# Kernel optimization log

Hardware: AMD Instinct MI355X
Metric: run time of the kernel (lower is better)

## Reference

```python
import jax, jax.numpy as jnp
import numpy as np

N_QUBITS = 9
N_LAYERS = 5
NUM_CLASSES = 10
BATCH = 4096
TWO_PI = 6.283185307179586


def _rx(theta):
    # RX(theta) = [[cos(t/2), -i sin(t/2)], [-i sin(t/2), cos(t/2)]]; theta scalar -> [2,2], [B] -> [B,2,2]
    c = jnp.cos(theta / 2).astype(jnp.complex64)
    s = ((-1j) * jnp.sin(theta / 2)).astype(jnp.complex64)
    return jnp.stack([jnp.stack([c, s], -1), jnp.stack([s, c], -1)], -2)


def _rot(phi, theta, omega):
    # PennyLane Rot = RZ(omega) @ RY(theta) @ RZ(phi)
    ct = jnp.cos(theta / 2)
    st = jnp.sin(theta / 2)
    a = jnp.exp(-0.5j * (phi + omega)) * ct
    b = -jnp.exp(0.5j * (phi - omega)) * st
    c = jnp.exp(-0.5j * (phi - omega)) * st
    d = jnp.exp(0.5j * (phi + omega)) * ct
    return jnp.stack([jnp.stack([a, b]), jnp.stack([c, d])]).astype(jnp.complex64)


def _apply1(state, gate, w):
    # state: [B] + [2]*9 (wire w lives on axis 1+w, wire 0 most significant as in PennyLane)
    s = jnp.moveaxis(state, 1 + w, -1)
    if gate.ndim == 3:  # per-sample gate (AngleEmbedding)
        s = jnp.einsum('bij,b...j->b...i', gate, s)
    else:
        s = jnp.einsum('ij,...j->...i', gate, s)
    return jnp.moveaxis(s, -1, 1 + w)


def _apply_crx(state, theta, ctrl, tgt):
    g = _rx(theta)  # [2,2]
    s = jnp.moveaxis(state, (1 + ctrl, 1 + tgt), (-2, -1))
    s1 = jnp.einsum('ij,...j->...i', g, s[..., 1, :])  # RX applied only where control bit = 1
    s = jnp.concatenate([s[..., :1, :], s1[..., None, :]], axis=-2)
    return jnp.moveaxis(s, (-2, -1), (1 + ctrl, 1 + tgt))


def _circuit(x, rot_w, crx_w):
    B = x.shape[0]
    state = jnp.zeros((B,) + (2,) * N_QUBITS, jnp.complex64)
    state = state.at[(slice(None),) + (0,) * N_QUBITS].set(1.0)  # |0...0>
    for n in range(N_LAYERS):
        for w in range(N_QUBITS):  # AngleEmbedding (RX) with per-sample angles
            state = _apply1(state, _rx(x[:, w]), w)
        for w in range(N_QUBITS):  # Rot gates
            state = _apply1(state, _rot(rot_w[n, w, 0], rot_w[n, w, 1], rot_w[n, w, 2]), w)
        for w in range(N_QUBITS):  # CRX ring entanglers
            state = _apply_crx(state, crx_w[n, w, 0], w, (w + 1) % N_QUBITS)
    probs = state.real ** 2 + state.imag ** 2  # [B] + [2]*9
    evs = []
    for w in range(N_QUBITS):
        other = tuple(a for a in range(1, N_QUBITS + 1) if a != 1 + w)
        p = probs.sum(axis=other)  # [B, 2]
        evs.append(p[:, 0] - p[:, 1])  # <Z_w>
    return jnp.stack(evs, axis=-1)  # [B, 9]


def setup_inputs() -> dict:
    key = jax.random.key(0)
    k0, k1, k2, k3 = jax.random.split(key, 4)
    x = jax.random.normal(k0, (BATCH, N_QUBITS), dtype=jnp.float32)
    rot_w = jax.random.uniform(k1, (N_LAYERS, N_QUBITS, 3), dtype=jnp.float32, minval=0.0, maxval=TWO_PI)
    crx_w = jax.random.uniform(k2, (N_LAYERS, N_QUBITS, 1), dtype=jnp.float32, minval=0.0, maxval=TWO_PI)
    fc_w = jax.random.normal(k3, (NUM_CLASSES, N_QUBITS), dtype=jnp.float32) * (1.0 / 3.0)
    fc_b = jnp.zeros((NUM_CLASSES,), dtype=jnp.float32)
    return {"x": x, "rot_w": rot_w, "crx_w": crx_w, "fc_w": fc_w, "fc_b": fc_b}


def reference(x, rot_w, crx_w, fc_w, fc_b):
    evs = _circuit(x, rot_w, crx_w)            # [B, 9] PauliZ expectation values
    logits = evs @ fc_w.T + fc_b               # [B, num_classes]
    return jax.nn.log_softmax(logits, axis=1)
```

## Files before the change

### kernel.cpp

```cpp
#include <hip/hip_runtime.h>
#include <math.h>

#define NQ 9
#define NL 5
#define NC 10

typedef float v2f __attribute__((ext_vector_type(2)));
typedef float v4f __attribute__((ext_vector_type(4)));

__device__ __forceinline__ v2f sp(float x) { v2f r; r.x = x; r.y = x; return r; }

__device__ __forceinline__ void plswap(float& a, float& b, int mask) {
    if (mask == 32) {
        auto r = __builtin_amdgcn_permlane32_swap(__float_as_int(a), __float_as_int(b), false, false);
        a = __int_as_float(r[0]); b = __int_as_float(r[1]);
    } else {
        auto r = __builtin_amdgcn_permlane16_swap(__float_as_int(a), __float_as_int(b), false, false);
        a = __int_as_float(r[0]); b = __int_as_float(r[1]);
    }
}
__device__ __forceinline__ void plswap2(v2f& a, v2f& b, int mask) {
    float ax = a.x, bx = b.x, ay = a.y, by = b.y;
    plswap(ax, bx, mask); plswap(ay, by, mask);
    a.x = ax; a.y = ay; b.x = bx; b.y = by;
}
__device__ __forceinline__ void state_swap(v2f (&xr)[4], v2f (&xi)[4], int mask) {
    plswap2(xr[0], xr[1], mask); plswap2(xr[2], xr[3], mask);
    plswap2(xi[0], xi[1], mask); plswap2(xi[2], xi[3], mask);
}

__device__ __forceinline__ void swpm(float x, int mask, float& hi, float& lo) {
    if (mask == 32) {
        auto r = __builtin_amdgcn_permlane32_swap(__float_as_int(x), __float_as_int(x), false, false);
        lo = __int_as_float(r[0]); hi = __int_as_float(r[1]);
    } else {
        auto r = __builtin_amdgcn_permlane16_swap(__float_as_int(x), __float_as_int(x), false, false);
        lo = __int_as_float(r[0]); hi = __int_as_float(r[1]);
    }
}

__device__ __forceinline__ float xmove(float x, int mask) {
    if (mask == 1)
        return __int_as_float(__builtin_amdgcn_update_dpp(0, __float_as_int(x), 0xB1, 0xF, 0xF, true));
    if (mask == 2)
        return __int_as_float(__builtin_amdgcn_update_dpp(0, __float_as_int(x), 0x4E, 0xF, 0xF, true));
    if (mask == 4) {
        int t = __builtin_amdgcn_update_dpp(0, __float_as_int(x), 0x104, 0xF, 0x5, false);
        t = __builtin_amdgcn_update_dpp(t, __float_as_int(x), 0x114, 0xF, 0xA, false);
        return __int_as_float(t);
    }
    return __int_as_float(__builtin_amdgcn_update_dpp(0, __float_as_int(x), 0x128, 0xF, 0xF, true));
}
__device__ __forceinline__ v2f xmv2(v2f v, int mask) {
    v2f r; r.x = xmove(v.x, mask); r.y = xmove(v.y, mask); return r;
}


#define HALF_U(A, c, s)                                               \
    float u00r = A.x*c + s*A.w,  u00i = A.y*c - s*A.z;                \
    float u01r = A.z*c + s*A.y,  u01i = A.w*c - s*A.x;

__device__ __forceinline__ void rot_pair(v2f (&xr)[4], v2f (&xi)[4],
                                         const float* __restrict__ m, float c, float s) {
    const v4f A = *(const v4f*)m;
    HALF_U(A, c, s)
#pragma unroll
    for (int p = 0; p < 4; p += 2) {
        const int q = p + 1;
        v2f a0r = xr[p], a0i = xi[p], a1r = xr[q], a1i = xi[q];
        xr[p] = sp(u00r)*a0r - sp(u00i)*a0i + sp(u01r)*a1r - sp(u01i)*a1i;
        xi[p] = sp(u00r)*a0i + sp(u00i)*a0r + sp(u01r)*a1i + sp(u01i)*a1r;
        xr[q] = sp(-u01r)*a0r - sp(u01i)*a0i + sp(u00r)*a1r + sp(u00i)*a1i;
        xi[q] = sp(-u01r)*a0i + sp(u01i)*a0r + sp(u00r)*a1i - sp(u00i)*a1r;
    }
}

template<int CB, int LB>
__device__ __forceinline__ void fusedC_cross(v2f (&xr)[4], v2f (&xi)[4],
                                             const float* __restrict__ m,
                                             float c, float s, int lane) {
    const v4f A0 = *(const v4f*)m;
    const v4f A1 = *(const v4f*)(m + 4);
    const bool ctrl = (lane >> CB) & 1;
    v4f A;
    A.x = ctrl ? A1.x : A0.x;  A.y = ctrl ? A1.y : A0.y;
    A.z = ctrl ? A1.z : A0.z;  A.w = ctrl ? A1.w : A0.w;
    HALF_U(A, c, s)
    const int bit = (lane >> LB) & 1;
    const float Csr = u00r,  Cpi = u01i;
    const float Csi = bit ? -u00i : u00i;
    const float Cpr = bit ? -u01r : u01r;
#pragma unroll
    for (int j = 0; j < 4; ++j) {
        v2f pr = xmv2(xr[j], 1 << LB);
        v2f pi = xmv2(xi[j], 1 << LB);
        v2f ar = xr[j], ai = xi[j];
        xr[j] = sp(Csr)*ar - sp(Csi)*ai + sp(Cpr)*pr - sp(Cpi)*pi;
        xi[j] = sp(Csr)*ai + sp(Csi)*ar + sp(Cpr)*pi + sp(Cpi)*pr;
    }
}

__device__ __forceinline__ void fusedC_j1(v2f (&xr)[4], v2f (&xi)[4],
                                          const float* __restrict__ m,
                                          float c, float s, int lane) {
    const v4f A0 = *(const v4f*)m;
    const v4f A1 = *(const v4f*)(m + 4);
    const bool ctrl = lane & 1;
    v4f A;
    A.x = ctrl ? A1.x : A0.x;  A.y = ctrl ? A1.y : A0.y;
    A.z = ctrl ? A1.z : A0.z;  A.w = ctrl ? A1.w : A0.w;
    HALF_U(A, c, s)
#pragma unroll
    for (int j = 0; j < 2; ++j) {
        const int q = j | 2;
        v2f a0r = xr[j], a0i = xi[j], a1r = xr[q], a1i = xi[q];
        xr[j] = sp(u00r)*a0r - sp(u00i)*a0i + sp(u01r)*a1r - sp(u01i)*a1i;
        xi[j] = sp(u00r)*a0i + sp(u00i)*a0r + sp(u01r)*a1i + sp(u01i)*a1r;
        xr[q] = sp(-u01r)*a0r - sp(u01i)*a0i + sp(u00r)*a1r + sp(u00i)*a1i;
        xi[q] = sp(-u01r)*a0i + sp(u01i)*a0r + sp(u00r)*a1i - sp(u00i)*a1r;
    }
}

__device__ __forceinline__ void rot_comp(v2f (&xr)[4], v2f (&xi)[4],
                                         const float* __restrict__ m, float c, float s) {
    const v4f A = *(const v4f*)m;
    HALF_U(A, c, s)
    v2f U0r = { u00r, -u01r }, U0i = { u00i,  u01i };
    v2f U1r = { u01r,  u00r }, U1i = { u01i, -u00i };
#pragma unroll
    for (int j = 0; j < 4; ++j) {
        v2f A0r = xr[j].xx, A0i = xi[j].xx, A1r = xr[j].yy, A1i = xi[j].yy;
        xr[j] = U0r*A0r - U0i*A0i + U1r*A1r - U1i*A1i;
        xi[j] = U0r*A0i + U0i*A0r + U1r*A1i + U1i*A1r;
    }
}

template<int CB, int M>
__device__ __forceinline__ void crx_dpp(v2f (&xr)[4], v2f (&xi)[4], float c, float s, int lane) {
    const bool ctrl = (lane >> CB) & 1;
    const float ce = ctrl ? c : 1.f;
    const float se = ctrl ? s : 0.f;
#pragma unroll
    for (int j = 0; j < 4; ++j) {
        v2f pr = xmv2(xr[j], M);
        v2f pi = xmv2(xi[j], M);
        xr[j] = sp(ce)*xr[j] + sp(se)*pi;
        xi[j] = sp(ce)*xi[j] - sp(se)*pr;
    }
}
__device__ __forceinline__ void crx_pair_s(v2f (&xr)[4], v2f (&xi)[4], float ce, float se) {
#pragma unroll
    for (int p = 0; p < 4; p += 2) {
        const int q = p + 1;
        v2f a0r = xr[p], a0i = xi[p], a1r = xr[q], a1i = xi[q];
        xr[p] = sp(ce)*a0r + sp(se)*a1i;
        xi[p] = sp(ce)*a0i - sp(se)*a1r;
        xr[q] = sp(ce)*a1r + sp(se)*a0i;
        xi[q] = sp(ce)*a1i - sp(se)*a0r;
    }
}
__device__ __forceinline__ void crx_pair_c(v2f (&xr)[4], v2f (&xi)[4], float c, float s) {
    const v2f cev = {1.f, c};
    const v2f sev = {0.f, s};
#pragma unroll
    for (int p = 0; p < 4; p += 2) {
        const int q = p + 1;
        v2f a0r = xr[p], a0i = xi[p], a1r = xr[q], a1i = xi[q];
        xr[p] = cev*a0r + sev*a1i;
        xi[p] = cev*a0i - sev*a1r;
        xr[q] = cev*a1r + sev*a0i;
        xi[q] = cev*a1i - sev*a0r;
    }
}
__device__ __forceinline__ void crx_l_j1(v2f (&xr)[4], v2f (&xi)[4], float c, float s, int lane) {
    const bool ctrl = lane & 1;
    const float ce = ctrl ? c : 1.f;
    const float se = ctrl ? s : 0.f;
#pragma unroll
    for (int j = 0; j < 2; ++j) {
        const int q = j | 2;
        v2f a0r = xr[j], a0i = xi[j], a1r = xr[q], a1i = xi[q];
        xr[j] = sp(ce)*a0r + sp(se)*a1i;
        xi[j] = sp(ce)*a0i - sp(se)*a1r;
        xr[q] = sp(ce)*a1r + sp(se)*a0i;
        xi[q] = sp(ce)*a1i - sp(se)*a0r;
    }
}
__device__ __forceinline__ void crx_j1_j0(v2f (&xr)[4], v2f (&xi)[4], float c, float s) {
    v2f a0r = xr[2], a0i = xi[2], a1r = xr[3], a1i = xi[3];
    xr[2] = sp(c)*a0r + sp(s)*a1i;
    xi[2] = sp(c)*a0i - sp(s)*a1r;
    xr[3] = sp(c)*a1r + sp(s)*a0i;
    xi[3] = sp(c)*a1i - sp(s)*a0r;
}
__device__ __forceinline__ void crx_j0_c(v2f (&xr)[4], v2f (&xi)[4], float c, float s) {
#pragma unroll
    for (int j = 1; j < 4; j += 2) {
        v2f vr = xr[j], vi = xi[j];
        xr[j] = sp(c)*vr + sp(s)*vi.yx;
        xi[j] = sp(c)*vi - sp(s)*vr.yx;
    }
}

__global__ __launch_bounds__(256) void qmlp_kernel(
    const float* __restrict__ x, const float* __restrict__ rot_w,
    const float* __restrict__ crx_w, const float* __restrict__ fc_w,
    const float* __restrict__ fc_b, float* __restrict__ out, int B)
{
    __shared__ __align__(16) float rotm[NL * NQ * 8];
    __shared__ __align__(16) float crxm[NL * NQ * 2];
    __shared__ float fcw[NC * NQ];
    __shared__ float fcbs[NC];

    const int tid = threadIdx.x;
    if (tid < NL * NQ) {
        const int n = tid / NQ, w = tid % NQ;
        const float phi = rot_w[tid * 3 + 0];
        const float th  = rot_w[tid * 3 + 1];
        const float om  = rot_w[tid * 3 + 2];
        float st, ct; sincosf(0.5f * th, &st, &ct);
        float spo, cpo; sincosf(0.5f * (phi + om), &spo, &cpo);
        float smo, cmo; sincosf(0.5f * (phi - om), &smo, &cmo);
        const float m00r =  ct * cpo, m00i = -ct * spo;
        const float m01r = -st * cmo, m01i = -st * smo;
        float* m = rotm + tid * 8;
        m[0] = m00r; m[1] = m00i; m[2] = m01r; m[3] = m01i;
        const int nb = n * NQ + (w + NQ - 1) % NQ;
        float sq, cq; sincosf(0.5f * crx_w[nb], &sq, &cq);
        m[4] = cq*m00r + sq*m01i;
        m[5] = cq*m00i + sq*m01r;
        m[6] = cq*m01r - sq*m00i;
        m[7] = cq*m01i - sq*m00r;
        float sc, cc; sincosf(0.5f * crx_w[tid], &sc, &cc);
        crxm[tid * 2 + 0] = cc; crxm[tid * 2 + 1] = sc;
    }
    if (tid < NC * NQ) fcw[tid] = fc_w[tid];
    if (tid < NC) fcbs[tid] = fc_b[tid];
    __syncthreads();

    const int lane = tid & 63;
    const int b = blockIdx.x * 4 + (tid >> 6);
    if (b >= B) return;

    float cx[NQ], sx[NQ];
#pragma unroll
    for (int w = 0; w < NQ; ++w) __sincosf(0.5f * x[b * NQ + w], &sx[w], &cx[w]);

    v2f xr[4], xi[4];

    {
        const float* M = rotm;
        float ar = 1.f, ai = 0.f;
#pragma unroll
        for (int w = 0; w < 6; ++w) {
            const v4f A = *(const v4f*)(M + w * 8);
            float c = cx[w], s = sx[w];
            HALF_U(A, c, s)
            int bit = (lane >> (5 - w)) & 1;
            float vr = bit ? -u01r : u00r;
            float vi = bit ?  u01i : u00i;
            float nr = ar * vr - ai * vi;
            float ni = ar * vi + ai * vr;
            ar = nr; ai = ni;
        }
        float vr67[2][2], vi67[2][2];
#pragma unroll
        for (int q = 0; q < 2; ++q) {
            const v4f A = *(const v4f*)(M + (6 + q) * 8);
            float c = cx[6 + q], s = sx[6 + q];
            HALF_U(A, c, s)
            vr67[q][0] = u00r;  vi67[q][0] = u00i;
            vr67[q][1] = -u01r; vi67[q][1] = u01i;
        }
        float t6r[2], t6i[2];
#pragma unroll
        for (int bb = 0; bb < 2; ++bb) {
            t6r[bb] = ar * vr67[0][bb] - ai * vi67[0][bb];
            t6i[bb] = ar * vi67[0][bb] + ai * vr67[0][bb];
        }
        float t67r[4], t67i[4];
#pragma unroll
        for (int j = 0; j < 4; ++j) {
            int b6 = j >> 1, b7 = j & 1;
            t67r[j] = t6r[b6] * vr67[1][b7] - t6i[b6] * vi67[1][b7];
            t67i[j] = t6r[b6] * vi67[1][b7] + t6i[b6] * vr67[1][b7];
        }
        {
            const v4f A = *(const v4f*)(M + 8 * 8);
            float c = cx[8], s = sx[8];
            HALF_U(A, c, s)
            v2f V8r = { u00r, -u01r };
            v2f V8i = { u00i,  u01i };
#pragma unroll
            for (int j = 0; j < 4; ++j) {
                xr[j] = sp(t67r[j])*V8r - sp(t67i[j])*V8i;
                xi[j] = sp(t67r[j])*V8i + sp(t67i[j])*V8r;
            }
        }
    }

    {
        const float* C = crxm;
        state_swap(xr, xi, 16);
        {
            const bool ctrl = (lane >> 5) & 1;
            crx_pair_s(xr, xi, ctrl ? C[0] : 1.f, ctrl ? C[1] : 0.f);
        }
        state_swap(xr, xi, 16);
        crx_dpp<4, 8>(xr, xi, C[2],  C[3],  lane);
        crx_dpp<3, 4>(xr, xi, C[4],  C[5],  lane);
        crx_dpp<2, 2>(xr, xi, C[6],  C[7],  lane);
        crx_dpp<1, 1>(xr, xi, C[8],  C[9],  lane);
        crx_l_j1     (xr, xi, C[10], C[11], lane);
        crx_j1_j0    (xr, xi, C[12], C[13]);
        crx_j0_c     (xr, xi, C[14], C[15]);
        state_swap(xr, xi, 32);
        crx_pair_c(xr, xi, C[16], C[17]);
    }

    for (int n = 1; n < NL; ++n) {
        const float* M = rotm + n * NQ * 8;
        const float* C = crxm + n * NQ * 2;
        rot_pair(xr, xi, M + 0 * 8, cx[0], sx[0]);
        state_swap(xr, xi, 32);
        state_swap(xr, xi, 16);
        rot_pair(xr, xi, M + 1 * 8, cx[1], sx[1]);
        {
            const bool ctrl = (lane >> 5) & 1;
            crx_pair_s(xr, xi, ctrl ? C[0] : 1.f, ctrl ? C[1] : 0.f);
        }
        state_swap(xr, xi, 16);
        fusedC_cross<4, 3>(xr, xi, M + 2 * 8, cx[2], sx[2], lane);
        fusedC_cross<3, 2>(xr, xi, M + 3 * 8, cx[3], sx[3], lane);
        fusedC_cross<2, 1>(xr, xi, M + 4 * 8, cx[4], sx[4], lane);
        fusedC_cross<1, 0>(xr, xi, M + 5 * 8, cx[5], sx[5], lane);
        fusedC_j1(xr, xi, M + 6 * 8, cx[6], sx[6], lane);
        rot_pair(xr, xi, M + 7 * 8, cx[7], sx[7]);
        crx_j1_j0(xr, xi, C[12], C[13]);
        rot_comp(xr, xi, M + 8 * 8, cx[8], sx[8]);
        crx_j0_c(xr, xi, C[14], C[15]);
        state_swap(xr, xi, 32);
        crx_pair_c(xr, xi, C[16], C[17]);
    }
    state_swap(xr, xi, 32);

    v2f P[4];
#pragma unroll
    for (int j = 0; j < 4; ++j) P[j] = xr[j]*xr[j] + xi[j]*xi[j];
    float ps[4];
#pragma unroll
    for (int j = 0; j < 4; ++j) ps[j] = P[j].x + P[j].y;
    float psum = ps[0] + ps[1] + ps[2] + ps[3];

    float t = psum;
    float d[6];
#pragma unroll
    for (int bb = 0; bb < 6; ++bb) {
        if (bb < 4) {
#pragma unroll
            for (int jj = 0; jj < 6; ++jj)
                if (jj < bb) d[jj] += xmove(d[jj], 1 << bb);
            float o = xmove(t, 1 << bb);
            d[bb] = ((lane >> bb) & 1) ? (o - t) : (t - o);
            t += o;
        } else {
#pragma unroll
            for (int jj = 0; jj < 6; ++jj)
                if (jj < bb) { float h, l; swpm(d[jj], 1 << bb, h, l); d[jj] = h + l; }
            float h, l; swpm(t, 1 << bb, h, l);
            d[bb] = l - h;
            t = h + l;
        }
    }
    float e6 = (ps[0] + ps[1]) - (ps[2] + ps[3]);
    float e7 = (ps[0] + ps[2]) - (ps[1] + ps[3]);
    float e8 = (P[0].x - P[0].y) + (P[1].x - P[1].y)
             + (P[2].x - P[2].y) + (P[3].x - P[3].y);
#pragma unroll
    for (int m = 1; m < 16; m <<= 1) {
        e6 += xmove(e6, m); e7 += xmove(e7, m); e8 += xmove(e8, m);
    }
    {
        float h, l;
        swpm(e6, 16, h, l); e6 = h + l;  swpm(e6, 32, h, l); e6 = h + l;
        swpm(e7, 16, h, l); e7 = h + l;  swpm(e7, 32, h, l); e7 = h + l;
        swpm(e8, 16, h, l); e8 = h + l;  swpm(e8, 32, h, l); e8 = h + l;
    }

    float ev[NQ];
#pragma unroll
    for (int w = 0; w < 6; ++w) ev[w] = d[5 - w];
    ev[6] = e6; ev[7] = e7; ev[8] = e8;

    float lval = -INFINITY;
    if (lane < NC) {
        float dd = fcbs[lane];
        const float* fw = fcw + lane * NQ;
#pragma unroll
        for (int w = 0; w < NQ; ++w) dd += ev[w] * fw[w];
        lval = dd;
    }
    float mx = lval;
    mx = fmaxf(mx, xmove(mx, 1));
    mx = fmaxf(mx, xmove(mx, 2));
    mx = fmaxf(mx, xmove(mx, 4));
    mx = fmaxf(mx, xmove(mx, 8));
    float e = (lane < NC) ? expf(lval - mx) : 0.f;
    float se = e;
    se += xmove(se, 1); se += xmove(se, 2); se += xmove(se, 4); se += xmove(se, 8);
    if (lane < NC) out[b * NC + lane] = lval - mx - logf(se);
}

extern "C" void kernel_launch(void* const* d_in, const int* in_sizes, int n_in,
                              void* d_out, int out_size, void* d_ws, size_t ws_size,
                              hipStream_t stream) {
    const float* x     = (const float*)d_in[0];
    const float* rot_w = (const float*)d_in[1];
    const float* crx_w = (const float*)d_in[2];
    const float* fc_w  = (const float*)d_in[3];
    const float* fc_b  = (const float*)d_in[4];
    float* out = (float*)d_out;
    const int B = in_sizes[0] / NQ;
    const int blocks = (B + 3) / 4;
    qmlp_kernel<<<blocks, 256, 0, stream>>>(x, rot_w, crx_w, fc_w, fc_b, out, B);
}
```

Before: 31.06 us.

## Process two batch samples per wavefront with interleaved state updates

Each wavefront now simulates two independent samples, keeping two register-resident state vectors and interleaving their gate, swap and reduction steps. The grid is halved to match. The aim is more instruction-level parallelism to hide DPP/permlane and ALU latency, and to amortise the per-block shared-memory setup over more samples. In exchange it doubles register pressure, which may lower occupancy, and leaves half as many wavefronts on the GPU. When B is odd, x is read out of bounds for the second sample (b1) even though its output write is guarded.

Result: no change. 30.88 us (-0.6%).

```diff
diff --git a/kernel.cpp b/kernel.cpp
--- a/kernel.cpp
+++ b/kernel.cpp
@@ -54,7 +54,6 @@
 __device__ __forceinline__ v2f xmv2(v2f v, int mask) {
     v2f r; r.x = xmove(v.x, mask); r.y = xmove(v.y, mask); return r;
 }
-
 
 #define HALF_U(A, c, s)                                               \
     float u00r = A.x*c + s*A.w,  u00i = A.y*c - s*A.z;                \
@@ -199,6 +198,57 @@
         v2f vr = xr[j], vi = xi[j];
         xr[j] = sp(c)*vr + sp(s)*vi.yx;
         xi[j] = sp(c)*vi - sp(s)*vr.yx;
+    }
+}
+
+__device__ __forceinline__ void init_state(v2f (&xr)[4], v2f (&xi)[4],
+                                           const float* __restrict__ M,
+                                           const float (&cx)[NQ], const float (&sx)[NQ],
+                                           int lane) {
+    float ar = 1.f, ai = 0.f;
+#pragma unroll
+    for (int w = 0; w < 6; ++w) {
+        const v4f A = *(const v4f*)(M + w * 8);
+        float c = cx[w], s = sx[w];
+        HALF_U(A, c, s)
+        int bit = (lane >> (5 - w)) & 1;
+        float vr = bit ? -u01r : u00r;
+        float vi = bit ?  u01i : u00i;
+        float nr = ar * vr - ai * vi;
+        float ni = ar * vi + ai * vr;
+        ar = nr; ai = ni;
+    }
+    float vr67[2][2], vi67[2][2];
+#pragma unroll
+    for (int q = 0; q < 2; ++q) {
+        const v4f A = *(const v4f*)(M + (6 + q) * 8);
+        float c = cx[6 + q], s = sx[6 + q];
+        HALF_U(A, c, s)
+        vr67[q][0] = u00r;  vi67[q][0] = u00i;
+        vr67[q][1] = -u01r; vi67[q][1] = u01i;
+    }
+    float t6r[2], t6i[2];
+#pragma unroll
+    for (int bb = 0; bb < 2; ++bb) {
+        t6r[bb] = ar * vr67[0][bb] - ai * vi67[0][bb];
+        t6i[bb] = ar * vi67[0][bb] + ai * vr67[0][bb];
+    }
+    float t67r[4], t67i[4];
+#pragma unroll
+    for (int j = 0; j < 4; ++j) {
+        int b6 = j >> 1, b7 = j & 1;
+        t67r[j] = t6r[b6] * vr67[1][b7] - t6i[b6] * vi67[1][b7];
+        t67i[j] = t6r[b6] * vi67[1][b7] + t6i[b6] * vr67[1][b7];
+    }
+    const v4f A = *(const v4f*)(M + 8 * 8);
+    float c = cx[8], s = sx[8];
+    HALF_U(A, c, s)
+    v2f V8r = { u00r, -u01r };
+    v2f V8i = { u00i,  u01i };
+#pragma unroll
+    for (int j = 0; j < 4; ++j) {
+        xr[j] = sp(t67r[j])*V8r - sp(t67i[j])*V8i;
+        xi[j] = sp(t67r[j])*V8i + sp(t67i[j])*V8r;
     }
 }
 
@@ -239,176 +289,179 @@
     __syncthreads();
 
     const int lane = tid & 63;
-    const int b = blockIdx.x * 4 + (tid >> 6);
-    if (b >= B) return;
-
-    float cx[NQ], sx[NQ];
-#pragma unroll
-    for (int w = 0; w < NQ; ++w) __sincosf(0.5f * x[b * NQ + w], &sx[w], &cx[w]);
-
-    v2f xr[4], xi[4];
-
-    {
-        const float* M = rotm;
-        float ar = 1.f, ai = 0.f;
-#pragma unroll
-        for (int w = 0; w < 6; ++w) {
-            const v4f A = *(const v4f*)(M + w * 8);
-            float c = cx[w], s = sx[w];
-            HALF_U(A, c, s)
-            int bit = (lane >> (5 - w)) & 1;
-            float vr = bit ? -u01r : u00r;
-            float vi = bit ?  u01i : u00i;
-            float nr = ar * vr - ai * vi;
-            float ni = ar * vi + ai * vr;
-            ar = nr; ai = ni;
-        }
-        float vr67[2][2], vi67[2][2];
-#pragma unroll
-        for (int q = 0; q < 2; ++q) {
-            const v4f A = *(const v4f*)(M + (6 + q) * 8);
-            float c = cx[6 + q], s = sx[6 + q];
-            HALF_U(A, c, s)
-            vr67[q][0] = u00r;  vi67[q][0] = u00i;
-            vr67[q][1] = -u01r; vi67[q][1] = u01i;
-        }
-        float t6r[2], t6i[2];
-#pragma unroll
-        for (int bb = 0; bb < 2; ++bb) {
-            t6r[bb] = ar * vr67[0][bb] - ai * vi67[0][bb];
-            t6i[bb] = ar * vi67[0][bb] + ai * vr67[0][bb];
-        }
-        float t67r[4], t67i[4];
-#pragma unroll
-        for (int j = 0; j < 4; ++j) {
-            int b6 = j >> 1, b7 = j & 1;
-            t67r[j] = t6r[b6] * vr67[1][b7] - t6i[b6] * vi67[1][b7];
-            t67i[j] = t6r[b6] * vi67[1][b7] + t6i[b6] * vr67[1][b7];
-        }
-        {
-            const v4f A = *(const v4f*)(M + 8 * 8);
-            float c = cx[8], s = sx[8];
-            HALF_U(A, c, s)
-            v2f V8r = { u00r, -u01r };
-            v2f V8i = { u00i,  u01i };
-#pragma unroll
-            for (int j = 0; j < 4; ++j) {
-                xr[j] = sp(t67r[j])*V8r - sp(t67i[j])*V8i;
-                xi[j] = sp(t67r[j])*V8i + sp(t67i[j])*V8r;
-            }
-        }
-    }
+    const int b0 = (blockIdx.x * 4 + (tid >> 6)) * 2;
+    const int b1 = b0 + 1;
+    if (b0 >= B) return;
+
+    float cxA[NQ], sxA[NQ], cxB[NQ], sxB[NQ];
+#pragma unroll
+    for (int w = 0; w < NQ; ++w) __sincosf(0.5f * x[b0 * NQ + w], &sxA[w], &cxA[w]);
+#pragma unroll
+    for (int w = 0; w < NQ; ++w) __sincosf(0.5f * x[b1 * NQ + w], &sxB[w], &cxB[w]);
+
+    v2f xrA[4], xiA[4], xrB[4], xiB[4];
+    init_state(xrA, xiA, rotm, cxA, sxA, lane);
+    init_state(xrB, xiB, rotm, cxB, sxB, lane);
 
     {
         const float* C = crxm;
-        state_swap(xr, xi, 16);
+        state_swap(xrA, xiA, 16);
+        state_swap(xrB, xiB, 16);
         {
             const bool ctrl = (lane >> 5) & 1;
-            crx_pair_s(xr, xi, ctrl ? C[0] : 1.f, ctrl ? C[1] : 0.f);
+            const float ce = ctrl ? C[0] : 1.f, se = ctrl ? C[1] : 0.f;
+            crx_pair_s(xrA, xiA, ce, se);
+            crx_pair_s(xrB, xiB, ce, se);
         }
-        state_swap(xr, xi, 16);
-        crx_dpp<4, 8>(xr, xi, C[2],  C[3],  lane);
-        crx_dpp<3, 4>(xr, xi, C[4],  C[5],  lane);
-        crx_dpp<2, 2>(xr, xi, C[6],  C[7],  lane);
-        crx_dpp<1, 1>(xr, xi, C[8],  C[9],  lane);
-        crx_l_j1     (xr, xi, C[10], C[11], lane);
-        crx_j1_j0    (xr, xi, C[12], C[13]);
-        crx_j0_c     (xr, xi, C[14], C[15]);
-        state_swap(xr, xi, 32);
-        crx_pair_c(xr, xi, C[16], C[17]);
+        state_swap(xrA, xiA, 16);
+        state_swap(xrB, xiB, 16);
+        crx_dpp<4, 8>(xrA, xiA, C[2],  C[3],  lane);  crx_dpp<4, 8>(xrB, xiB, C[2],  C[3],  lane);
+        crx_dpp<3, 4>(xrA, xiA, C[4],  C[5],  lane);  crx_dpp<3, 4>(xrB, xiB, C[4],  C[5],  lane);
+        crx_dpp<2, 2>(xrA, xiA, C[6],  C[7],  lane);  crx_dpp<2, 2>(xrB, xiB, C[6],  C[7],  lane);
+        crx_dpp<1, 1>(xrA, xiA, C[8],  C[9],  lane);  crx_dpp<1, 1>(xrB, xiB, C[8],  C[9],  lane);
+        crx_l_j1     (xrA, xiA, C[10], C[11], lane);  crx_l_j1     (xrB, xiB, C[10], C[11], lane);
+        crx_j1_j0    (xrA, xiA, C[12], C[13]);        crx_j1_j0    (xrB, xiB, C[12], C[13]);
+        crx_j0_c     (xrA, xiA, C[14], C[15]);        crx_j0_c     (xrB, xiB, C[14], C[15]);
+        state_swap(xrA, xiA, 32);
+        state_swap(xrB, xiB, 32);
+        crx_pair_c(xrA, xiA, C[16], C[17]);
+        crx_pair_c(xrB, xiB, C[16], C[17]);
     }
 
     for (int n = 1; n < NL; ++n) {
         const float* M = rotm + n * NQ * 8;
         const float* C = crxm + n * NQ * 2;
-        rot_pair(xr, xi, M + 0 * 8, cx[0], sx[0]);
-        state_swap(xr, xi, 32);
-        state_swap(xr, xi, 16);
-        rot_pair(xr, xi, M + 1 * 8, cx[1], sx[1]);
+        rot_pair(xrA, xiA, M + 0 * 8, cxA[0], sxA[0]);
+        rot_pair(xrB, xiB, M + 0 * 8, cxB[0], sxB[0]);
+        state_swap(xrA, xiA, 32);
+        state_swap(xrB, xiB, 32);
+        state_swap(xrA, xiA, 16);
+        state_swap(xrB, xiB, 16);
+        rot_pair(xrA, xiA, M + 1 * 8, cxA[1], sxA[1]);
+        rot_pair(xrB, xiB, M + 1 * 8, cxB[1], sxB[1]);
         {
             const bool ctrl = (lane >> 5) & 1;
-            crx_pair_s(xr, xi, ctrl ? C[0] : 1.f, ctrl ? C[1] : 0.f);
+            const float ce = ctrl ? C[0] : 1.f, se = ctrl ? C[1] : 0.f;
+            crx_pair_s(xrA, xiA, ce, se);
+            crx_pair_s(xrB, xiB, ce, se);
         }
-        state_swap(xr, xi, 16);
-        fusedC_cross<4, 3>(xr, xi, M + 2 * 8, cx[2], sx[2], lane);
-        fusedC_cross<3, 2>(xr, xi, M + 3 * 8, cx[3], sx[3], lane);
-        fusedC_cross<2, 1>(xr, xi, M + 4 * 8, cx[4], sx[4], lane);
-        fusedC_cross<1, 0>(xr, xi, M + 5 * 8, cx[5], sx[5], lane);
-        fusedC_j1(xr, xi, M + 6 * 8, cx[6], sx[6], lane);
-        rot_pair(xr, xi, M + 7 * 8, cx[7], sx[7]);
-        crx_j1_j0(xr, xi, C[12], C[13]);
-        rot_comp(xr, xi, M + 8 * 8, cx[8], sx[8]);
-        crx_j0_c(xr, xi, C[14], C[15]);
-        state_swap(xr, xi, 32);
-        crx_pair_c(xr, xi, C[16], C[17]);
-    }
-    state_swap(xr, xi, 32);
-
-    v2f P[4];
-#pragma unroll
-    for (int j = 0; j < 4; ++j) P[j] = xr[j]*xr[j] + xi[j]*xi[j];
-    float ps[4];
-#pragma unroll
-    for (int j = 0; j < 4; ++j) ps[j] = P[j].x + P[j].y;
-    float psum = ps[0] + ps[1] + ps[2] + ps[3];
-
-    float t = psum;
-    float d[6];
+        state_swap(xrA, xiA, 16);
+        state_swap(xrB, xiB, 16);
+        fusedC_cross<4, 3>(xrA, xiA, M + 2 * 8, cxA[2], sxA[2], lane);
+        fusedC_cross<4, 3>(xrB, xiB, M + 2 * 8, cxB[2], sxB[2], lane);
+        fusedC_cross<3, 2>(xrA, xiA, M + 3 * 8, cxA[3], sxA[3], lane);
+        fusedC_cross<3, 2>(xrB, xiB, M + 3 * 8, cxB[3], sxB[3], lane);
+        fusedC_cross<2, 1>(xrA, xiA, M + 4 * 8, cxA[4], sxA[4], lane);
+        fusedC_cross<2, 1>(xrB, xiB, M + 4 * 8, cxB[4], sxB[4], lane);
+        fusedC_cross<1, 0>(xrA, xiA, M + 5 * 8, cxA[5], sxA[5], lane);
+        fusedC_cross<1, 0>(xrB, xiB, M + 5 * 8, cxB[5], sxB[5], lane);
+        fusedC_j1(xrA, xiA, M + 6 * 8, cxA[6], sxA[6], lane);
+        fusedC_j1(xrB, xiB, M + 6 * 8, cxB[6], sxB[6], lane);
+        rot_pair(xrA, xiA, M + 7 * 8, cxA[7], sxA[7]);
+        rot_pair(xrB, xiB, M + 7 * 8, cxB[7], sxB[7]);
+        crx_j1_j0(xrA, xiA, C[12], C[13]);
+        crx_j1_j0(xrB, xiB, C[12], C[13]);
+        rot_comp(xrA, xiA, M + 8 * 8, cxA[8], sxA[8]);
+        rot_comp(xrB, xiB, M + 8 * 8, cxB[8], sxB[8]);
+        crx_j0_c(xrA, xiA, C[14], C[15]);
+        crx_j0_c(xrB, xiB, C[14], C[15]);
+        state_swap(xrA, xiA, 32);
+        state_swap(xrB, xiB, 32);
+        crx_pair_c(xrA, xiA, C[16], C[17]);
+        crx_pair_c(xrB, xiB, C[16], C[17]);
+    }
+    state_swap(xrA, xiA, 32);
+    state_swap(xrB, xiB, 32);
+
+    v2f PA[4], PB[4];
+#pragma unroll
+    for (int j = 0; j < 4; ++j) { PA[j] = xrA[j]*xrA[j] + xiA[j]*xiA[j];
+                                  PB[j] = xrB[j]*xrB[j] + xiB[j]*xiB[j]; }
+    float psA[4], psB[4];
+#pragma unroll
+    for (int j = 0; j < 4; ++j) { psA[j] = PA[j].x + PA[j].y; psB[j] = PB[j].x + PB[j].y; }
+    float tA = psA[0] + psA[1] + psA[2] + psA[3];
+    float tB = psB[0] + psB[1] + psB[2] + psB[3];
+
+    float dA[6], dB[6];
 #pragma unroll
     for (int bb = 0; bb < 6; ++bb) {
         if (bb < 4) {
 #pragma unroll
             for (int jj = 0; jj < 6; ++jj)
-                if (jj < bb) d[jj] += xmove(d[jj], 1 << bb);
-            float o = xmove(t, 1 << bb);
-            d[bb] = ((lane >> bb) & 1) ? (o - t) : (t - o);
-            t += o;
+                if (jj < bb) { dA[jj] += xmove(dA[jj], 1 << bb); dB[jj] += xmove(dB[jj], 1 << bb); }
+            float oA = xmove(tA, 1 << bb);
+            float oB = xmove(tB, 1 << bb);
+            bool hibit = (lane >> bb) & 1;
+            dA[bb] = hibit ? (oA - tA) : (tA - oA);
+            dB[bb] = hibit ? (oB - tB) : (tB - oB);
+            tA += oA; tB += oB;
         } else {
 #pragma unroll
             for (int jj = 0; jj < 6; ++jj)
-                if (jj < bb) { float h, l; swpm(d[jj], 1 << bb, h, l); d[jj] = h + l; }
-            float h, l; swpm(t, 1 << bb, h, l);
-            d[bb] = l - h;
-            t = h + l;
+                if (jj < bb) {
+                    float h, l;
+                    swpm(dA[jj], 1 << bb, h, l); dA[jj] = h + l;
+                    swpm(dB[jj], 1 << bb, h, l); dB[jj] = h + l;
+                }
+            float hA, lA, hB, lB;
+            swpm(tA, 1 << bb, hA, lA);
+            swpm(tB, 1 << bb, hB, lB);
+            dA[bb] = lA - hA; tA = hA + lA;
+            dB[bb] = lB - hB; tB = hB + lB;
         }
     }
-    float e6 = (ps[0] + ps[1]) - (ps[2] + ps[3]);
-    float e7 = (ps[0] + ps[2]) - (ps[1] + ps[3]);
-    float e8 = (P[0].x - P[0].y) + (P[1].x - P[1].y)
-             + (P[2].x - P[2].y) + (P[3].x - P[3].y);
+    float e6A = (psA[0] + psA[1]) - (psA[2] + psA[3]);
+    float e7A = (psA[0] + psA[2]) - (psA[1] + psA[3]);
+    float e8A = (PA[0].x - PA[0].y) + (PA[1].x - PA[1].y) + (PA[2].x - PA[2].y) + (PA[3].x - PA[3].y);
+    float e6B = (psB[0] + psB[1]) - (psB[2] + psB[3]);
+    float e7B = (psB[0] + psB[2]) - (psB[1] + psB[3]);
+    float e8B = (PB[0].x - PB[0].y) + (PB[1].x - PB[1].y) + (PB[2].x - PB[2].y) + (PB[3].x - PB[3].y);
 #pragma unroll
     for (int m = 1; m < 16; m <<= 1) {
-        e6 += xmove(e6, m); e7 += xmove(e7, m); e8 += xmove(e8, m);
+        e6A += xmove(e6A, m); e7A += xmove(e7A, m); e8A += xmove(e8A, m);
+        e6B += xmove(e6B, m); e7B += xmove(e7B, m); e8B += xmove(e8B, m);
     }
     {
         float h, l;
-        swpm(e6, 16, h, l); e6 = h + l;  swpm(e6, 32, h, l); e6 = h + l;
-        swpm(e7, 16, h, l); e7 = h + l;  swpm(e7, 32, h, l); e7 = h + l;
-        swpm(e8, 16, h, l); e8 = h + l;  swpm(e8, 32, h, l); e8 = h + l;
-    }
-
-    float ev[NQ];
-#pragma unroll
-    for (int w = 0; w < 6; ++w) ev[w] = d[5 - w];
-    ev[6] = e6; ev[7] = e7; ev[8] = e8;
-
-    float lval = -INFINITY;
+        swpm(e6A, 16, h, l); e6A = h + l;  swpm(e6A, 32, h, l); e6A = h + l;
+        swpm(e7A, 16, h, l); e7A = h + l;  swpm(e7A, 32, h, l); e7A = h + l;
+        swpm(e8A, 16, h, l); e8A = h + l;  swpm(e8A, 32, h, l); e8A = h + l;
+        swpm(e6B, 16, h, l); e6B = h + l;  swpm(e6B, 32, h, l); e6B = h + l;
+        swpm(e7B, 16, h, l); e7B = h + l;  swpm(e7B, 32, h, l); e7B = h + l;
+        swpm(e8B, 16, h, l); e8B = h + l;  swpm(e8B, 32, h, l); e8B = h + l;
+    }
+
+    float evA[NQ], evB[NQ];
+#pragma unroll
+    for (int w = 0; w < 6; ++w) { evA[w] = dA[5 - w]; evB[w] = dB[5 - w]; }
+    evA[6] = e6A; evA[7] = e7A; evA[8] = e8A;
+    evB[6] = e6B; evB[7] = e7B; evB[8] = e8B;
+
+    float lvA = -INFINITY, lvB = -INFINITY;
     if (lane < NC) {
-        float dd = fcbs[lane];
+        float a = fcbs[lane], c2 = a;
         const float* fw = fcw + lane * NQ;
 #pragma unroll
-        for (int w = 0; w < NQ; ++w) dd += ev[w] * fw[w];
-        lval = dd;
-    }
-    float mx = lval;
-    mx = fmaxf(mx, xmove(mx, 1));
-    mx = fmaxf(mx, xmove(mx, 2));
-    mx = fmaxf(mx, xmove(mx, 4));
-    mx = fmaxf(mx, xmove(mx, 8));
-    float e = (lane < NC) ? expf(lval - mx) : 0.f;
-    float se = e;
-    se += xmove(se, 1); se += xmove(se, 2); se += xmove(se, 4); se += xmove(se, 8);
-    if (lane < NC) out[b * NC + lane] = lval - mx - logf(se);
+        for (int w = 0; w < NQ; ++w) { a += evA[w] * fw[w]; c2 += evB[w] * fw[w]; }
+        lvA = a; lvB = c2;
+    }
+    float mxA = lvA, mxB = lvB;
+    mxA = fmaxf(mxA, xmove(mxA, 1)); mxB = fmaxf(mxB, xmove(mxB, 1));
+    mxA = fmaxf(mxA, xmove(mxA, 2)); mxB = fmaxf(mxB, xmove(mxB, 2));
+    mxA = fmaxf(mxA, xmove(mxA, 4)); mxB = fmaxf(mxB, xmove(mxB, 4));
+    mxA = fmaxf(mxA, xmove(mxA, 8)); mxB = fmaxf(mxB, xmove(mxB, 8));
+    float eA = (lane < NC) ? expf(lvA - mxA) : 0.f;
+    float eB = (lane < NC) ? expf(lvB - mxB) : 0.f;
+    float seA = eA, seB = eB;
+    seA += xmove(seA, 1); seB += xmove(seB, 1);
+    seA += xmove(seA, 2); seB += xmove(seB, 2);
+    seA += xmove(seA, 4); seB += xmove(seB, 4);
+    seA += xmove(seA, 8); seB += xmove(seB, 8);
+    if (lane < NC) {
+        out[b0 * NC + lane] = lvA - mxA - logf(seA);
+        if (b1 < B) out[b1 * NC + lane] = lvB - mxB - logf(seB);
+    }
 }
 
 extern "C" void kernel_launch(void* const* d_in, const int* in_sizes, int n_in,
@@ -421,6 +474,7 @@
     const float* fc_b  = (const float*)d_in[4];
     float* out = (float*)d_out;
     const int B = in_sizes[0] / NQ;
-    const int blocks = (B + 3) / 4;
+    const int nw = (B + 1) / 2;
+    const int blocks = (nw + 3) / 4;
     qmlp_kernel<<<blocks, 256, 0, stream>>>(x, rot_w, crx_w, fc_w, fc_b, out, B);
 }
```

## Fold CRX gates into adjacent rotation matrices via precomputed dual matrices

Applied to the files above, without the earlier changes.

Removes separate CRX passes inside the layer loop by folding them into neighbouring rotation gates. It uses dual (control-selected) precomputed matrices for wires 1, 7 and 8, and merges the last CRX of the previous layer into the next layer's first RX angle. This cuts the per-layer VALU work and register shuffles for the state. The change relies on a host- or setup-side precompute of the doubled rotation matrices (m+4 slots) for those wires, and on RX angle composition holding per control half. If that precompute does not exist, the results will be wrong.

New measurement: 30.17 us. 2.9% less time.

```diff
diff --git a/kernel.cpp b/kernel.cpp
--- a/kernel.cpp
+++ b/kernel.cpp
@@ -55,23 +55,78 @@
     v2f r; r.x = xmove(v.x, mask); r.y = xmove(v.y, mask); return r;
 }
 
-
 #define HALF_U(A, c, s)                                               \
     float u00r = A.x*c + s*A.w,  u00i = A.y*c - s*A.z;                \
     float u01r = A.z*c + s*A.y,  u01i = A.w*c - s*A.x;
 
-__device__ __forceinline__ void rot_pair(v2f (&xr)[4], v2f (&xi)[4],
-                                         const float* __restrict__ m, float c, float s) {
+#define PAIR_BODY(p, q)                                                       \
+    {                                                                         \
+        v2f a0r = xr[p], a0i = xi[p], a1r = xr[q], a1i = xi[q];               \
+        xr[p] = sp(u00r)*a0r - sp(u00i)*a0i + sp(u01r)*a1r - sp(u01i)*a1i;    \
+        xi[p] = sp(u00r)*a0i + sp(u00i)*a0r + sp(u01r)*a1i + sp(u01i)*a1r;    \
+        xr[q] = sp(-u01r)*a0r - sp(u01i)*a0i + sp(u00r)*a1r + sp(u00i)*a1i;   \
+        xi[q] = sp(-u01r)*a0i + sp(u01i)*a0r + sp(u00r)*a1i - sp(u00i)*a1r;   \
+    }
+
+__device__ __forceinline__ void rot_pair_dual(v2f (&xr)[4], v2f (&xi)[4],
+                                              const float* __restrict__ m, float c, float s) {
+    const v4f A0 = *(const v4f*)m;
+    const v4f A1 = *(const v4f*)(m + 4);
+    { HALF_U(A0, c, s) PAIR_BODY(0, 1) }
+    { HALF_U(A1, c, s) PAIR_BODY(2, 3) }
+}
+
+__device__ __forceinline__ void rot_pair_sel(v2f (&xr)[4], v2f (&xi)[4],
+                                             const float* __restrict__ m, float c, float s,
+                                             bool ctrl) {
+    const v4f A0 = *(const v4f*)m;
+    const v4f A1 = *(const v4f*)(m + 4);
+    v4f A;
+    A.x = ctrl ? A1.x : A0.x;  A.y = ctrl ? A1.y : A0.y;
+    A.z = ctrl ? A1.z : A0.z;  A.w = ctrl ? A1.w : A0.w;
+    HALF_U(A, c, s)
+    PAIR_BODY(0, 1)
+    PAIR_BODY(2, 3)
+}
+
+__device__ __forceinline__ void rot_pair_v2(v2f (&xr)[4], v2f (&xi)[4],
+                                            const float* __restrict__ m, v2f c, v2f s) {
     const v4f A = *(const v4f*)m;
-    HALF_U(A, c, s)
+    v2f u00r = sp(A.x)*c + s*sp(A.w);
+    v2f u00i = sp(A.y)*c - s*sp(A.z);
+    v2f u01r = sp(A.z)*c + s*sp(A.y);
+    v2f u01i = sp(A.w)*c - s*sp(A.x);
 #pragma unroll
     for (int p = 0; p < 4; p += 2) {
         const int q = p + 1;
         v2f a0r = xr[p], a0i = xi[p], a1r = xr[q], a1i = xi[q];
-        xr[p] = sp(u00r)*a0r - sp(u00i)*a0i + sp(u01r)*a1r - sp(u01i)*a1i;
-        xi[p] = sp(u00r)*a0i + sp(u00i)*a0r + sp(u01r)*a1i + sp(u01i)*a1r;
-        xr[q] = sp(-u01r)*a0r - sp(u01i)*a0i + sp(u00r)*a1r + sp(u00i)*a1i;
-        xi[q] = sp(-u01r)*a0i + sp(u01i)*a0r + sp(u00r)*a1i - sp(u00i)*a1r;
+        xr[p] = u00r*a0r - u00i*a0i + u01r*a1r - u01i*a1i;
+        xi[p] = u00r*a0i + u00i*a0r + u01r*a1i + u01i*a1r;
+        xr[q] = -u01r*a0r - u01i*a0i + u00r*a1r + u00i*a1i;
+        xi[q] = -u01r*a0i + u01i*a0r + u00r*a1i - u00i*a1r;
+    }
+}
+
+__device__ __forceinline__ void rot_comp_dual(v2f (&xr)[4], v2f (&xi)[4],
+                                              const float* __restrict__ m, float c, float s) {
+    const v4f A0v = *(const v4f*)m;
+    const v4f A1v = *(const v4f*)(m + 4);
+    v2f U0r0, U0i0, U1r0, U1i0, U0r1, U0i1, U1r1, U1i1;
+    { HALF_U(A0v, c, s)
+      U0r0 = (v2f){ u00r, -u01r }; U0i0 = (v2f){ u00i,  u01i };
+      U1r0 = (v2f){ u01r,  u00r }; U1i0 = (v2f){ u01i, -u00i }; }
+    { HALF_U(A1v, c, s)
+      U0r1 = (v2f){ u00r, -u01r }; U0i1 = (v2f){ u00i,  u01i };
+      U1r1 = (v2f){ u01r,  u00r }; U1i1 = (v2f){ u01i, -u00i }; }
+#pragma unroll
+    for (int j = 0; j < 4; ++j) {
+        v2f U0r = (j & 1) ? U0r1 : U0r0;
+        v2f U0i = (j & 1) ? U0i1 : U0i0;
+        v2f U1r = (j & 1) ? U1r1 : U1r0;
+        v2f U1i = (j & 1) ? U1i1 : U1i0;
+        v2f A0r = xr[j].xx, A0i = xi[j].xx, A1r = xr[j].yy, A1i = xi[j].yy;
+        xr[j] = U0r*A0r - U0i*A0i + U1r*A1r - U1i*A1i;
+        xi[j] = U0r*A0i + U0i*A0r + U1r*A1i + U1i*A1r;
     }
 }
 
@@ -118,20 +173,6 @@
         xi[j] = sp(u00r)*a0i + sp(u00i)*a0r + sp(u01r)*a1i + sp(u01i)*a1r;
         xr[q] = sp(-u01r)*a0r - sp(u01i)*a0i + sp(u00r)*a1r + sp(u00i)*a1i;
         xi[q] = sp(-u01r)*a0i + sp(u01i)*a0r + sp(u00r)*a1i - sp(u00i)*a1r;
-    }
-}
-
-__device__ __forceinline__ void rot_comp(v2f (&xr)[4], v2f (&xi)[4],
-                                         const float* __restrict__ m, float c, float s) {
-    const v4f A = *(const v4f*)m;
-    HALF_U(A, c, s)
-    v2f U0r = { u00r, -u01r }, U0i = { u00i,  u01i };
-    v2f U1r = { u01r,  u00r }, U1i = { u01i, -u00i };
-#pragma unroll
-    for (int j = 0; j < 4; ++j) {
-        v2f A0r = xr[j].xx, A0i = xi[j].xx, A1r = xr[j].yy, A1i = xi[j].yy;
-        xr[j] = U0r*A0r - U0i*A0i + U1r*A1r - U1i*A1i;
-        xi[j] = U0r*A0i + U0i*A0r + U1r*A1i + U1i*A1r;
     }
 }
 
@@ -315,33 +356,34 @@
         crx_j1_j0    (xr, xi, C[12], C[13]);
         crx_j0_c     (xr, xi, C[14], C[15]);
         state_swap(xr, xi, 32);
-        crx_pair_c(xr, xi, C[16], C[17]);
     }
 
     for (int n = 1; n < NL; ++n) {
-        const float* M = rotm + n * NQ * 8;
-        const float* C = crxm + n * NQ * 2;
-        rot_pair(xr, xi, M + 0 * 8, cx[0], sx[0]);
+        const float* M  = rotm + n * NQ * 8;
+        const float* C  = crxm + n * NQ * 2;
+        const float* Cp = crxm + (n - 1) * NQ * 2;
+        {
+            v2f cv, sv;
+            cv.x = cx[0];
+            sv.x = sx[0];
+            cv.y = cx[0]*Cp[16] - sx[0]*Cp[17];
+            sv.y = sx[0]*Cp[16] + cx[0]*Cp[17];
+            rot_pair_v2(xr, xi, M + 0 * 8, cv, sv);
+        }
         state_swap(xr, xi, 32);
         state_swap(xr, xi, 16);
-        rot_pair(xr, xi, M + 1 * 8, cx[1], sx[1]);
-        {
-            const bool ctrl = (lane >> 5) & 1;
-            crx_pair_s(xr, xi, ctrl ? C[0] : 1.f, ctrl ? C[1] : 0.f);
-        }
+        rot_pair_sel(xr, xi, M + 1 * 8, cx[1], sx[1], (lane >> 5) & 1);
         state_swap(xr, xi, 16);
         fusedC_cross<4, 3>(xr, xi, M + 2 * 8, cx[2], sx[2], lane);
         fusedC_cross<3, 2>(xr, xi, M + 3 * 8, cx[3], sx[3], lane);
         fusedC_cross<2, 1>(xr, xi, M + 4 * 8, cx[4], sx[4], lane);
         fusedC_cross<1, 0>(xr, xi, M + 5 * 8, cx[5], sx[5], lane);
         fusedC_j1(xr, xi, M + 6 * 8, cx[6], sx[6], lane);
-        rot_pair(xr, xi, M + 7 * 8, cx[7], sx[7]);
-        crx_j1_j0(xr, xi, C[12], C[13]);
-        rot_comp(xr, xi, M + 8 * 8, cx[8], sx[8]);
-        crx_j0_c(xr, xi, C[14], C[15]);
+        rot_pair_dual(xr, xi, M + 7 * 8, cx[7], sx[7]);
+        rot_comp_dual(xr, xi, M + 8 * 8, cx[8], sx[8]);
         state_swap(xr, xi, 32);
-        crx_pair_c(xr, xi, C[16], C[17]);
-    }
+    }
+    crx_pair_c(xr, xi, crxm[4 * NQ * 2 + 16], crxm[4 * NQ * 2 + 17]);
     state_swap(xr, xi, 32);
 
     v2f P[4];
```
